# Kernel optimization log

Measured on AMD Instinct MI355X. Metric: run time of the kernel, lower is better.

Reference implementation:

```python
import jax, jax.numpy as jnp
import numpy as np

B, T, C, H = 2, 2048, 1024, 16
D = C // H  # head_dim = 64

def setup_inputs() -> dict:
    key = jax.random.key(0)
    k1, k2, k3 = jax.random.split(key, 3)
    x = jax.random.normal(k1, (B, T, C), dtype=jnp.float32)
    W_attn = jax.random.normal(k2, (C, 3 * C), dtype=jnp.float32) * (1.0 / np.sqrt(C))
    W_proj = jax.random.normal(k3, (C, C), dtype=jnp.float32) * (1.0 / np.sqrt(C))
    return {"x": x, "W_attn": W_attn, "W_proj": W_proj}

def reference(x, W_attn, W_proj):
    b, t, c = x.shape
    qkv = x @ W_attn                       # [B,T,3C]
    q, k, v = jnp.split(qkv, 3, axis=-1)
    # [B,T,C] -> [B,H,T,D]
    q = q.reshape(b, t, H, D).transpose(0, 2, 1, 3)
    k = k.reshape(b, t, H, D).transpose(0, 2, 1, 3)
    v = v.reshape(b, t, H, D).transpose(0, 2, 1, 3)
    scale = 1.0 / np.sqrt(D).astype(np.float32)
    att = jnp.einsum('bhqd,bhkd->bhqk', q, k) * scale   # [B,H,T,T]
    causal = jnp.tril(jnp.ones((t, t), dtype=bool))
    att = jnp.where(causal[None, None], att, -jnp.inf)
    att = jax.nn.softmax(att, axis=-1)
    y = jnp.einsum('bhqk,bhkd->bhqd', att, v)           # [B,H,T,D]
    y = y.transpose(0, 2, 1, 3).reshape(b, t, c)        # [B,T,C]
    return y @ W_proj
```

## Files before the change

### kernel.cpp

```cpp
#include <hip/hip_runtime.h>
#include <hip/hip_bf16.h>
#include <cstdint>
#include <cstddef>
#include <cmath>

typedef __attribute__((ext_vector_type(8))) short short8v;
typedef __attribute__((ext_vector_type(4))) float f32x4;
typedef __attribute__((ext_vector_type(4))) unsigned short ushort4v;

__device__ __forceinline__ unsigned short f2bf(float f) {
  union { float f; uint32_t u; } v; v.f = f;
  uint32_t u = v.u;
  return (unsigned short)((u + 0x7fffu + ((u >> 16) & 1u)) >> 16);
}

__device__ __forceinline__ float bf2f(unsigned short u) {
  union { uint32_t u; float f; } v; v.u = ((uint32_t)u) << 16; return v.f;
}

__device__ __forceinline__ uint32_t pack2bf(float a, float b) {
  __hip_bfloat162 h = __float22bfloat162_rn(make_float2(a, b));
  union { __hip_bfloat162 h; uint32_t u; } c; c.h = h; return c.u;
}

__device__ __forceinline__ void load_lds_16B(const void* g, void* l) {
  __builtin_amdgcn_global_load_lds((const __attribute__((address_space(1))) void*)g,
                                   (__attribute__((address_space(3))) void*)l, 16, 0, 0);
}

__global__ __launch_bounds__(256) void cvt_bf16_kernel(const float* __restrict__ src,
                                                       unsigned short* __restrict__ dst,
                                                       int n8) {
  int i = blockIdx.x * 256 + threadIdx.x;
  if (i >= n8) return;
  const float4* s4 = (const float4*)src + (size_t)i * 2;
  float4 f0 = s4[0], f1 = s4[1];
  short8v o;
  o[0] = (short)f2bf(f0.x); o[1] = (short)f2bf(f0.y);
  o[2] = (short)f2bf(f0.z); o[3] = (short)f2bf(f0.w);
  o[4] = (short)f2bf(f1.x); o[5] = (short)f2bf(f1.y);
  o[6] = (short)f2bf(f1.z); o[7] = (short)f2bf(f1.w);
  *(short8v*)(dst + (size_t)i * 8) = o;
}

__global__ __launch_bounds__(256) void transpose_bf16_kernel(const float* __restrict__ W,
                                                             unsigned short* __restrict__ WT,
                                                             int K, int N) {
  __shared__ float tile[64][65];
  int n0 = blockIdx.x * 64, k0 = blockIdx.y * 64;
  int tid = threadIdx.x;
#pragma unroll
  for (int i = 0; i < 4; ++i) {
    int idx = i * 256 + tid;
    int r = idx >> 4, c4 = (idx & 15) * 4;
    float4 v = *(const float4*)(W + (size_t)(k0 + r) * N + n0 + c4);
    tile[r][c4] = v.x; tile[r][c4 + 1] = v.y; tile[r][c4 + 2] = v.z; tile[r][c4 + 3] = v.w;
  }
  __syncthreads();
#pragma unroll
  for (int i = 0; i < 4; ++i) {
    int idx = i * 256 + tid;
    int nr = idx >> 4, k4 = (idx & 15) * 4;
    ushort4 o;
    o.x = f2bf(tile[k4 + 0][nr]);
    o.y = f2bf(tile[k4 + 1][nr]);
    o.z = f2bf(tile[k4 + 2][nr]);
    o.w = f2bf(tile[k4 + 3][nr]);
    *(ushort4*)(WT + (size_t)(n0 + nr) * K + k0 + k4) = o;
  }
}

__global__ __launch_bounds__(256) void transpose_v_kernel(const unsigned short* __restrict__ qkv,
                                                          unsigned short* __restrict__ VT) {
  int bid = blockIdx.x;
  int b = bid >> 9, h = (bid >> 5) & 15, tc = bid & 31;
  __shared__ unsigned short tile[64][68];
  int tid = threadIdx.x;
  const unsigned short* src = qkv + (size_t)(b * 2048 + tc * 64) * 3072 + 2048 + h * 64;
#pragma unroll
  for (int p = 0; p < 4; ++p) {
    int idx = p * 256 + tid;
    int r = idx >> 4, c4 = (idx & 15) * 4;
    *(ushort4*)&tile[r][c4] = *(const ushort4*)(src + (size_t)r * 3072 + c4);
  }
  __syncthreads();
  unsigned short* dst = VT + (size_t)(b * 16 + h) * 64 * 2048 + tc * 64;
#pragma unroll
  for (int p = 0; p < 4; ++p) {
    int idx = p * 256 + tid;
    int d = idx >> 4, k = idx & 15;
    int t4 = k * 4;
    int c4 = ((k >> 3) << 5) | ((k & 3) << 3) | (k & 4);
    ushort4 o;
    o.x = tile[t4][d]; o.y = tile[t4 + 1][d]; o.z = tile[t4 + 2][d]; o.w = tile[t4 + 3][d];
    *(ushort4*)(dst + (size_t)d * 2048 + c4) = o;
  }
}

template <int BF16OUT>
__global__ __launch_bounds__(256) void gemm_bt_kernel(const unsigned short* __restrict__ A,
                                                      const unsigned short* __restrict__ BT,
                                                      void* __restrict__ Cout,
                                                      int M, int N, int K) {
  __shared__ __align__(16) char lds[32768];
  char* As = lds;
  char* Bs = lds + 16384;

  int nbn = N >> 7;
  int nwg = gridDim.x;
  int wg = blockIdx.x;
  int per = nwg >> 3;
  int swz = (wg & 7) * per + (wg >> 3);
  int tm = swz / nbn, tn = swz % nbn;

  int tid = threadIdx.x;
  int wid = tid >> 6, lane = tid & 63;
  int l15 = lane & 15, lhi = lane >> 4;
  int wm = wid >> 1, wn = wid & 1;

  const unsigned short* Abase = A + (size_t)(tm * 128) * K;
  const unsigned short* Bbase = BT + (size_t)(tn * 128) * K;

  size_t ofs[4];
#pragma unroll
  for (int i = 0; i < 4; ++i) {
    int row = i * 32 + (tid >> 3);
    int ss = (tid & 7) ^ (row & 7);
    ofs[i] = (size_t)row * K + ss * 8;
  }

  f32x4 acc[4][4] = {};

  for (int kt = 0; kt < K; kt += 64) {
    __syncthreads();
#pragma unroll
    for (int i = 0; i < 4; ++i)
      load_lds_16B(Abase + ofs[i] + kt, As + i * 4096 + tid * 16);
#pragma unroll
    for (int i = 0; i < 4; ++i)
      load_lds_16B(Bbase + ofs[i] + kt, Bs + i * 4096 + tid * 16);
    __syncthreads();

#pragma unroll
    for (int ks = 0; ks < 2; ++ks) {
      short8v af[4], bfr[4];
#pragma unroll
      for (int mi = 0; mi < 4; ++mi) {
        int row = wm * 64 + mi * 16 + l15;
        int ss = (ks * 4 + lhi) ^ (row & 7);
        af[mi] = *(const short8v*)(As + row * 128 + ss * 16);
      }
#pragma unroll
      for (int ni = 0; ni < 4; ++ni) {
        int row = wn * 64 + ni * 16 + l15;
        int ss = (ks * 4 + lhi) ^ (row & 7);
        bfr[ni] = *(const short8v*)(Bs + row * 128 + ss * 16);
      }
#pragma unroll
      for (int mi = 0; mi < 4; ++mi)
#pragma unroll
        for (int ni = 0; ni < 4; ++ni)
          acc[mi][ni] = __builtin_amdgcn_mfma_f32_16x16x32_bf16(af[mi], bfr[ni], acc[mi][ni], 0, 0, 0);
    }
  }

#pragma unroll
  for (int mi = 0; mi < 4; ++mi)
#pragma unroll
    for (int ni = 0; ni < 4; ++ni)
#pragma unroll
      for (int r = 0; r < 4; ++r) {
        int row = tm * 128 + wm * 64 + mi * 16 + lhi * 4 + r;
        int col = tn * 128 + wn * 64 + ni * 16 + l15;
        float v = acc[mi][ni][r];
        if (BF16OUT)
          ((unsigned short*)Cout)[(size_t)row * N + col] = f2bf(v);
        else
          ((float*)Cout)[(size_t)row * N + col] = v;
      }
}


__device__ __forceinline__ short8v scale_q(short8v q) {
  short8v r;
#pragma unroll
  for (int j = 0; j < 8; ++j)
    r[j] = (short)f2bf(bf2f((unsigned short)q[j]) * 0.18033688f);
  return r;
}

__device__ __forceinline__ void mask_diag(f32x4 s[4], int q_abs, int k0, int lhi) {
#pragma unroll
  for (int ni = 0; ni < 4; ++ni)
#pragma unroll
    for (int r = 0; r < 4; ++r) {
      int kv = k0 + ni * 16 + lhi * 4 + r;
      if (kv > q_abs) s[ni][r] = -1e30f;
    }
}

__device__ __forceinline__ void exp_sum(f32x4 s[4], float& rs) {
#pragma unroll
  for (int ni = 0; ni < 4; ++ni)
#pragma unroll
    for (int r = 0; r < 4; ++r) {
      float p = exp2f(s[ni][r] - 8.0f);
      s[ni][r] = p;
      rs += p;
    }
}

__device__ __forceinline__ void repack_pa(const f32x4 s[4], short8v pa[2]) {
#pragma unroll
  for (int ks = 0; ks < 2; ++ks) {
    union { uint32_t u[4]; short8v v; } pk;
    pk.u[0] = pack2bf(s[2 * ks][0], s[2 * ks][1]);
    pk.u[1] = pack2bf(s[2 * ks][2], s[2 * ks][3]);
    pk.u[2] = pack2bf(s[2 * ks + 1][0], s[2 * ks + 1][1]);
    pk.u[3] = pack2bf(s[2 * ks + 1][2], s[2 * ks + 1][3]);
    pa[ks] = pk.v;
  }
}

__global__ __launch_bounds__(256, 2) void attn_kernel(const unsigned short* __restrict__ qkv,
                                                      const unsigned short* __restrict__ VT,
                                                      unsigned short* __restrict__ yb) {
  const int T = 2048, LD = 3072;
  int bid = blockIdx.x;
  int xcd = bid & 7, ii = bid >> 3;
  int bh = xcd * 4 + (ii & 3);
  int j = ii >> 2;
  int b = bh >> 4, h = bh & 15;
  int qtA = j, qtB = 31 - j;

  int tid = threadIdx.x;
  int wid = tid >> 6, lane = tid & 63;
  int l15 = lane & 15, lhi = lane >> 4;

  __shared__ __align__(16) char Ks[4][8192];
  __shared__ __align__(16) char Vt[4][8192];

  int qrowA = qtA * 64 + wid * 16 + l15;
  int qrowB = qtB * 64 + wid * 16 + l15;
  const unsigned short* qpA = qkv + (size_t)(b * T + qrowA) * LD + h * 64;
  const unsigned short* qpB = qkv + (size_t)(b * T + qrowB) * LD + h * 64;
  short8v qfA[2], qfB[2];
  qfA[0] = scale_q(*(const short8v*)(qpA + lhi * 8));
  qfA[1] = scale_q(*(const short8v*)(qpA + 32 + lhi * 8));
  qfB[0] = scale_q(*(const short8v*)(qpB + lhi * 8));
  qfB[1] = scale_q(*(const short8v*)(qpB + 32 + lhi * 8));

  const unsigned short* kbase = qkv + (size_t)b * T * LD + 1024 + h * 64;
  const unsigned short* vtbase = VT + (size_t)(b * 16 + h) * 64 * 2048;

  f32x4 oA[4] = {}, oB[4] = {};
  float lA = 0.f, lB = 0.f;
  int q_absA = qtA * 64 + wid * 16 + l15;
  int q_absB = qtB * 64 + wid * 16 + l15;

  int ntA64 = qtA + 1, ntB64 = qtB + 1;
  int nSuper = (ntB64 + 1) >> 1;

  auto stageK = [&](int s) {
#pragma unroll
    for (int i2 = 0; i2 < 2; ++i2) {
      int row = i2 * 32 + (tid >> 3);
      int ss = (tid & 7) ^ (row & 7);
      load_lds_16B(kbase + (size_t)(s * 64 + row) * LD + ss * 8, Ks[s & 3] + i2 * 4096 + tid * 16);
    }
  };
  auto stageV = [&](int s) {
#pragma unroll
    for (int i2 = 0; i2 < 2; ++i2) {
      int row = i2 * 32 + (tid >> 3);
      int ss = (tid & 7) ^ (row & 7);
      load_lds_16B(vtbase + (size_t)row * 2048 + s * 64 + ss * 8, Vt[s & 3] + i2 * 4096 + tid * 16);
    }
  };

  stageK(0); stageV(0);
  stageK(1); stageV(1);
  __syncthreads();

  for (int its = 0; its < nSuper; ++its) {
    int sub0 = 2 * its, sub1 = sub0 + 1;
    int k0 = sub0 * 64;
    bool actB1 = sub1 < ntB64;
    bool actA0 = sub0 < ntA64;
    bool actA1 = sub1 < ntA64;
    int p0 = sub0 + 2, p1 = sub0 + 3;
    bool pf0 = p0 < ntB64, pf1 = p1 < ntB64;

    if (pf0) { stageK(p0); stageV(p0); }
    if (pf1) { stageK(p1); stageV(p1); }

    const char* K0 = Ks[sub0 & 3];
    const char* K1 = Ks[sub1 & 3];

    f32x4 sB0[4] = {}, sB1[4] = {}, sA0[4] = {}, sA1[4] = {};
    __builtin_amdgcn_s_setprio(1);
#pragma unroll
    for (int ks = 0; ks < 2; ++ks)
#pragma unroll
      for (int ni = 0; ni < 4; ++ni) {
        int row = ni * 16 + l15;
        int sl = (ks * 4 + lhi) ^ (row & 7);
        short8v kf = *(const short8v*)(K0 + row * 128 + sl * 16);
        sB0[ni] = __builtin_amdgcn_mfma_f32_16x16x32_bf16(kf, qfB[ks], sB0[ni], 0, 0, 0);
        if (actA0) sA0[ni] = __builtin_amdgcn_mfma_f32_16x16x32_bf16(kf, qfA[ks], sA0[ni], 0, 0, 0);
      }
    if (actB1) {
#pragma unroll
      for (int ks = 0; ks < 2; ++ks)
#pragma unroll
        for (int ni = 0; ni < 4; ++ni) {
          int row = ni * 16 + l15;
          int sl = (ks * 4 + lhi) ^ (row & 7);
          short8v kf = *(const short8v*)(K1 + row * 128 + sl * 16);
          sB1[ni] = __builtin_amdgcn_mfma_f32_16x16x32_bf16(kf, qfB[ks], sB1[ni], 0, 0, 0);
          if (actA1) sA1[ni] = __builtin_amdgcn_mfma_f32_16x16x32_bf16(kf, qfA[ks], sA1[ni], 0, 0, 0);
        }
    }
    __builtin_amdgcn_s_setprio(0);

    if (sub0 == qtB) mask_diag(sB0, q_absB, k0, lhi);
    if (sub1 == qtB) mask_diag(sB1, q_absB, k0 + 64, lhi);
    {
      float rs = 0.f;
      exp_sum(sB0, rs);
      if (actB1) exp_sum(sB1, rs);
      rs += __shfl_xor(rs, 16);
      rs += __shfl_xor(rs, 32);
      lB += rs;
    }
    if (actA0) {
      if (sub0 == qtA) mask_diag(sA0, q_absA, k0, lhi);
      if (sub1 == qtA) mask_diag(sA1, q_absA, k0 + 64, lhi);
      float rs = 0.f;
      exp_sum(sA0, rs);
      if (actA1) exp_sum(sA1, rs);
      rs += __shfl_xor(rs, 16);
      rs += __shfl_xor(rs, 32);
      lA += rs;
    }

    short8v paB0[2], paB1[2], paA0[2], paA1[2];
    repack_pa(sB0, paB0);
    if (actB1) repack_pa(sB1, paB1);
    if (actA0) repack_pa(sA0, paA0);
    if (actA1) repack_pa(sA1, paA1);

    const char* V0 = Vt[sub0 & 3];
    const char* V1 = Vt[sub1 & 3];
    __builtin_amdgcn_s_setprio(1);
#pragma unroll
    for (int ks = 0; ks < 2; ++ks)
#pragma unroll
      for (int nd = 0; nd < 4; ++nd) {
        int d = nd * 16 + l15;
        int slv = (ks * 4 + lhi) ^ (d & 7);
        short8v bv = *(const short8v*)(V0 + d * 128 + slv * 16);
        oB[nd] = __builtin_amdgcn_mfma_f32_16x16x32_bf16(paB0[ks], bv, oB[nd], 0, 0, 0);
        if (actA0) oA[nd] = __builtin_amdgcn_mfma_f32_16x16x32_bf16(paA0[ks], bv, oA[nd], 0, 0, 0);
      }
    if (actB1) {
#pragma unroll
      for (int ks = 0; ks < 2; ++ks)
#pragma unroll
        for (int nd = 0; nd < 4; ++nd) {
          int d = nd * 16 + l15;
          int slv = (ks * 4 + lhi) ^ (d & 7);
          short8v bv = *(const short8v*)(V1 + d * 128 + slv * 16);
          oB[nd] = __builtin_amdgcn_mfma_f32_16x16x32_bf16(paB1[ks], bv, oB[nd], 0, 0, 0);
          if (actA1) oA[nd] = __builtin_amdgcn_mfma_f32_16x16x32_bf16(paA1[ks], bv, oA[nd], 0, 0, 0);
        }
    }
    __builtin_amdgcn_s_setprio(0);

    __syncthreads();
  }

#pragma unroll
  for (int r = 0; r < 4; ++r) {
    float lrB = __shfl(lB, lhi * 4 + r);
    float lrA = __shfl(lA, lhi * 4 + r);
    float invB = 1.0f / lrB;
    float invA = 1.0f / lrA;
    int qB = qtB * 64 + wid * 16 + lhi * 4 + r;
    int qA = qtA * 64 + wid * 16 + lhi * 4 + r;
#pragma unroll
    for (int nd = 0; nd < 4; ++nd) {
      yb[(size_t)(b * T + qB) * 1024 + h * 64 + nd * 16 + l15] = f2bf(oB[nd][r] * invB);
      yb[(size_t)(b * T + qA) * 1024 + h * 64 + nd * 16 + l15] = f2bf(oA[nd][r] * invA);
    }
  }
}

extern "C" void kernel_launch(void* const* d_in, const int* in_sizes, int n_in,
                              void* d_out, int out_size, void* d_ws, size_t ws_size,
                              hipStream_t stream) {
  const float* x = (const float*)d_in[0];
  const float* Wa = (const float*)d_in[1];
  const float* Wp = (const float*)d_in[2];
  float* out = (float*)d_out;

  char* ws = (char*)d_ws;
  unsigned short* xb  = (unsigned short*)(ws);
  unsigned short* VT  = (unsigned short*)(ws);
  unsigned short* WaT = (unsigned short*)(ws + (size_t)(8u  << 20));
  unsigned short* WpT = (unsigned short*)(ws + (size_t)(14u << 20));
  unsigned short* qkv = (unsigned short*)(ws + (size_t)(16u << 20));
  unsigned short* yb  = (unsigned short*)(ws + (size_t)(40u << 20));

  cvt_bf16_kernel<<<2048, 256, 0, stream>>>(x, xb, 524288);
  transpose_bf16_kernel<<<dim3(48, 16), 256, 0, stream>>>(Wa, WaT, 1024, 3072);
  transpose_bf16_kernel<<<dim3(16, 16), 256, 0, stream>>>(Wp, WpT, 1024, 1024);
  gemm_bt_kernel<1><<<dim3(768), 256, 0, stream>>>(xb, WaT, qkv, 4096, 3072, 1024);
  transpose_v_kernel<<<dim3(1024), 256, 0, stream>>>(qkv, VT);
  attn_kernel<<<dim3(512), 256, 0, stream>>>(qkv, VT, yb);
  gemm_bt_kernel<0><<<dim3(256), 256, 0, stream>>>(yb, WpT, out, 4096, 1024, 1024);
}
```

Measured before the change: 120.4 us.

## Compute softmax row sums via MFMA with ones and use 64-row output GEMM

The attention kernel no longer sums exponentials with scalar adds and cross-lane shuffles. It accumulates row sums by multiplying the bf16 probability tiles by a ones vector on the matrix cores, which also yields per-row sums directly in the output layout. The fixed -8 exponent offset is removed, which risks overflow if scores grow large. The output projection now uses a new 64x128-tile GEMM with 512 workgroups instead of 256, for better occupancy across CUs, at the cost of less reuse per tile and no double buffering.

```diff
diff --git a/kernel.cpp b/kernel.cpp
--- a/kernel.cpp
+++ b/kernel.cpp
@@ -180,6 +180,89 @@
       }
 }
 
+__global__ __launch_bounds__(256) void gemm_bt64_kernel(const unsigned short* __restrict__ A,
+                                                        const unsigned short* __restrict__ BT,
+                                                        float* __restrict__ Cout,
+                                                        int M, int N, int K) {
+  __shared__ __align__(16) char lds[24576];
+  char* As = lds;
+  char* Bs = lds + 8192;
+
+  int nbn = N >> 7;
+  int nwg = gridDim.x;
+  int wg = blockIdx.x;
+  int per = nwg >> 3;
+  int swz = (wg & 7) * per + (wg >> 3);
+  int tm = swz / nbn, tn = swz % nbn;
+
+  int tid = threadIdx.x;
+  int wid = tid >> 6, lane = tid & 63;
+  int l15 = lane & 15, lhi = lane >> 4;
+
+  const unsigned short* Abase = A + (size_t)(tm * 64) * K;
+  const unsigned short* Bbase = BT + (size_t)(tn * 128) * K;
+
+  size_t ofsA[2], ofsB[4];
+#pragma unroll
+  for (int i = 0; i < 2; ++i) {
+    int row = i * 32 + (tid >> 3);
+    int ss = (tid & 7) ^ (row & 7);
+    ofsA[i] = (size_t)row * K + ss * 8;
+  }
+#pragma unroll
+  for (int i = 0; i < 4; ++i) {
+    int row = i * 32 + (tid >> 3);
+    int ss = (tid & 7) ^ (row & 7);
+    ofsB[i] = (size_t)row * K + ss * 8;
+  }
+
+  f32x4 acc[4][2] = {};
+
+  for (int kt = 0; kt < K; kt += 64) {
+    __syncthreads();
+#pragma unroll
+    for (int i = 0; i < 2; ++i)
+      load_lds_16B(Abase + ofsA[i] + kt, As + i * 4096 + tid * 16);
+#pragma unroll
+    for (int i = 0; i < 4; ++i)
+      load_lds_16B(Bbase + ofsB[i] + kt, Bs + i * 4096 + tid * 16);
+    __syncthreads();
+
+#pragma unroll
+    for (int ks = 0; ks < 2; ++ks) {
+      short8v af[4], bfr[2];
+#pragma unroll
+      for (int mi = 0; mi < 4; ++mi) {
+        int row = mi * 16 + l15;
+        int ss = (ks * 4 + lhi) ^ (row & 7);
+        af[mi] = *(const short8v*)(As + row * 128 + ss * 16);
+      }
+#pragma unroll
+      for (int ni = 0; ni < 2; ++ni) {
+        int row = wid * 32 + ni * 16 + l15;
+        int ss = (ks * 4 + lhi) ^ (row & 7);
+        bfr[ni] = *(const short8v*)(Bs + row * 128 + ss * 16);
+      }
+#pragma unroll
+      for (int mi = 0; mi < 4; ++mi)
+#pragma unroll
+        for (int ni = 0; ni < 2; ++ni)
+          acc[mi][ni] = __builtin_amdgcn_mfma_f32_16x16x32_bf16(af[mi], bfr[ni], acc[mi][ni], 0, 0, 0);
+    }
+  }
+
+#pragma unroll
+  for (int mi = 0; mi < 4; ++mi)
+#pragma unroll
+    for (int ni = 0; ni < 2; ++ni)
+#pragma unroll
+      for (int r = 0; r < 4; ++r) {
+        int row = tm * 64 + mi * 16 + lhi * 4 + r;
+        int col = tn * 128 + wid * 32 + ni * 16 + l15;
+        Cout[(size_t)row * N + col] = acc[mi][ni][r];
+      }
+}
+
 
 __device__ __forceinline__ short8v scale_q(short8v q) {
   short8v r;
@@ -199,15 +282,12 @@
     }
 }
 
-__device__ __forceinline__ void exp_sum(f32x4 s[4], float& rs) {
+__device__ __forceinline__ void exp_p(f32x4 s[4]) {
 #pragma unroll
   for (int ni = 0; ni < 4; ++ni)
 #pragma unroll
-    for (int r = 0; r < 4; ++r) {
-      float p = exp2f(s[ni][r] - 8.0f);
-      s[ni][r] = p;
-      rs += p;
-    }
+    for (int r = 0; r < 4; ++r)
+      s[ni][r] = exp2f(s[ni][r]);
 }
 
 __device__ __forceinline__ void repack_pa(const f32x4 s[4], short8v pa[2]) {
@@ -240,6 +320,10 @@
   __shared__ __align__(16) char Ks[4][8192];
   __shared__ __align__(16) char Vt[4][8192];
 
+  union { uint32_t u[4]; short8v v; } ob;
+  ob.u[0] = ob.u[1] = ob.u[2] = ob.u[3] = 0x3F803F80u;
+  const short8v onesv = ob.v;
+
   int qrowA = qtA * 64 + wid * 16 + l15;
   int qrowB = qtB * 64 + wid * 16 + l15;
   const unsigned short* qpA = qkv + (size_t)(b * T + qrowA) * LD + h * 64;
@@ -254,7 +338,7 @@
   const unsigned short* vtbase = VT + (size_t)(b * 16 + h) * 64 * 2048;
 
   f32x4 oA[4] = {}, oB[4] = {};
-  float lA = 0.f, lB = 0.f;
+  f32x4 lfA = {}, lfB = {};
   int q_absA = qtA * 64 + wid * 16 + l15;
   int q_absB = qtB * 64 + wid * 16 + l15;
 
@@ -325,23 +409,13 @@
 
     if (sub0 == qtB) mask_diag(sB0, q_absB, k0, lhi);
     if (sub1 == qtB) mask_diag(sB1, q_absB, k0 + 64, lhi);
-    {
-      float rs = 0.f;
-      exp_sum(sB0, rs);
-      if (actB1) exp_sum(sB1, rs);
-      rs += __shfl_xor(rs, 16);
-      rs += __shfl_xor(rs, 32);
-      lB += rs;
-    }
+    exp_p(sB0);
+    if (actB1) exp_p(sB1);
     if (actA0) {
       if (sub0 == qtA) mask_diag(sA0, q_absA, k0, lhi);
       if (sub1 == qtA) mask_diag(sA1, q_absA, k0 + 64, lhi);
-      float rs = 0.f;
-      exp_sum(sA0, rs);
-      if (actA1) exp_sum(sA1, rs);
-      rs += __shfl_xor(rs, 16);
-      rs += __shfl_xor(rs, 32);
-      lA += rs;
+      exp_p(sA0);
+      if (actA1) exp_p(sA1);
     }
 
     short8v paB0[2], paB1[2], paA0[2], paA1[2];
@@ -363,6 +437,11 @@
         oB[nd] = __builtin_amdgcn_mfma_f32_16x16x32_bf16(paB0[ks], bv, oB[nd], 0, 0, 0);
         if (actA0) oA[nd] = __builtin_amdgcn_mfma_f32_16x16x32_bf16(paA0[ks], bv, oA[nd], 0, 0, 0);
       }
+#pragma unroll
+    for (int ks = 0; ks < 2; ++ks) {
+      lfB = __builtin_amdgcn_mfma_f32_16x16x32_bf16(paB0[ks], onesv, lfB, 0, 0, 0);
+      if (actA0) lfA = __builtin_amdgcn_mfma_f32_16x16x32_bf16(paA0[ks], onesv, lfA, 0, 0, 0);
+    }
     if (actB1) {
 #pragma unroll
       for (int ks = 0; ks < 2; ++ks)
@@ -374,6 +453,11 @@
           oB[nd] = __builtin_amdgcn_mfma_f32_16x16x32_bf16(paB1[ks], bv, oB[nd], 0, 0, 0);
           if (actA1) oA[nd] = __builtin_amdgcn_mfma_f32_16x16x32_bf16(paA1[ks], bv, oA[nd], 0, 0, 0);
         }
+#pragma unroll
+      for (int ks = 0; ks < 2; ++ks) {
+        lfB = __builtin_amdgcn_mfma_f32_16x16x32_bf16(paB1[ks], onesv, lfB, 0, 0, 0);
+        if (actA1) lfA = __builtin_amdgcn_mfma_f32_16x16x32_bf16(paA1[ks], onesv, lfA, 0, 0, 0);
+      }
     }
     __builtin_amdgcn_s_setprio(0);
 
@@ -382,10 +466,8 @@
 
 #pragma unroll
   for (int r = 0; r < 4; ++r) {
-    float lrB = __shfl(lB, lhi * 4 + r);
-    float lrA = __shfl(lA, lhi * 4 + r);
-    float invB = 1.0f / lrB;
-    float invA = 1.0f / lrA;
+    float invB = 1.0f / lfB[r];
+    float invA = 1.0f / lfA[r];
     int qB = qtB * 64 + wid * 16 + lhi * 4 + r;
     int qA = qtA * 64 + wid * 16 + lhi * 4 + r;
 #pragma unroll
@@ -418,5 +500,5 @@
   gemm_bt_kernel<1><<<dim3(768), 256, 0, stream>>>(xb, WaT, qkv, 4096, 3072, 1024);
   transpose_v_kernel<<<dim3(1024), 256, 0, stream>>>(qkv, VT);
   attn_kernel<<<dim3(512), 256, 0, stream>>>(qkv, VT, yb);
-  gemm_bt_kernel<0><<<dim3(256), 256, 0, stream>>>(yb, WpT, out, 4096, 1024, 1024);
-}
+  gemm_bt64_kernel<<<dim3(512), 256, 0, stream>>>(yb, WpT, out, 4096, 1024, 1024);
+}
```

Measured after the change: 115.9 us. 3.7% less time.
